# Optimization experiments

Measured on AMD Instinct MI355X. Metric: run time of the kernel, lower is better.

## Reference

```python
import jax, jax.numpy as jnp
import numpy as np

E = 1024  # embedding_dim
H = 64    # head_size

def setup_inputs() -> dict:
    key = jax.random.key(0)
    k1, k2, k3, k4 = jax.random.split(key, 4)
    x = jax.random.normal(k1, (4, 4096, E), dtype=jnp.float32)
    # nn.Linear(E, H, bias=False) weights have shape [H, E]; y = x @ W.T
    s = 1.0 / np.sqrt(E)
    Wq = jax.random.normal(k2, (H, E), dtype=jnp.float32) * s
    Wk = jax.random.normal(k3, (H, E), dtype=jnp.float32) * s
    Wv = jax.random.normal(k4, (H, E), dtype=jnp.float32) * s
    return {"x": x, "Wq": Wq, "Wk": Wk, "Wv": Wv}

def reference(x, Wq, Wk, Wv):
    B, T, E_ = x.shape
    q = jnp.einsum('bte,he->bth', x, Wq)
    k = jnp.einsum('bte,he->bth', x, Wk)
    v = jnp.einsum('bte,he->bth', x, Wv)
    # NOTE: original scales by sqrt(embedding_dim), not head_size
    scores = jnp.einsum('bqh,bkh->bqk', q, k) / jnp.sqrt(jnp.asarray(E_, x.dtype))
    causal = jnp.tril(jnp.ones((T, T), dtype=bool))
    scores = jnp.where(causal, scores, -jnp.inf)
    weights = jax.nn.softmax(scores, axis=-1)
    return jnp.einsum('bqk,bkh->bqh', weights, v)
```

## Files before the change

### kernel.cpp

```cpp
#include <hip/hip_runtime.h>
#include <stdint.h>

typedef __bf16 bf16x8 __attribute__((ext_vector_type(8)));
typedef float  f32x4  __attribute__((ext_vector_type(4)));

#define E_DIM 1024
#define H_DIM 64
#define T_SEQ 4096
#define B_BAT 4
#define M_TOT (B_BAT * T_SEQ)

__device__ __forceinline__ uint32_t f2bf1(float f) {
    uint32_t u = __float_as_uint(f);
    return (u + 0x7FFFu + ((u >> 16) & 1u)) >> 16;
}
__device__ __forceinline__ uint32_t f2bf2(float lo, float hi) {
    return f2bf1(lo) | (f2bf1(hi) << 16);
}
__device__ __forceinline__ bf16x8 ldfrag(const ushort* p) {
    return __builtin_bit_cast(bf16x8, *(const uint4*)p);
}

__global__ __launch_bounds__(256) void wcvt(const float* __restrict__ Wq,
                                            const float* __restrict__ Wk,
                                            const float* __restrict__ Wv,
                                            ushort* __restrict__ Wfm) {
    int g = blockIdx.x * 256 + threadIdx.x;
    int n = g >> 7;
    int k8 = g & 127;
    const float* src = (n < 64) ? (Wq + (size_t)n * E_DIM)
                     : (n < 128) ? (Wk + (size_t)(n - 64) * E_DIM)
                     : (Wv + (size_t)(n - 128) * E_DIM);
    float sc = (n < 64) ? 0.03125f : 1.0f;
    float4 a = *(const float4*)(src + k8 * 8);
    float4 b = *(const float4*)(src + k8 * 8 + 4);
    uint4 o;
    o.x = f2bf2(a.x * sc, a.y * sc); o.y = f2bf2(a.z * sc, a.w * sc);
    o.z = f2bf2(b.x * sc, b.y * sc); o.w = f2bf2(b.z * sc, b.w * sc);
    int s = k8 >> 3, kc = (k8 >> 2) & 1, qd = k8 & 3;
    int nt = n >> 4, lm = n & 15;
    int lane = qd * 16 + lm;
    *(uint4*)(Wfm + (((size_t)(s * 12 + nt) * 2 + kc) * 64 + lane) * 8) = o;
}

__global__ __launch_bounds__(256, 2) void qkv(const float* __restrict__ x,
                                              const ushort* __restrict__ Wfm,
                                              ushort* __restrict__ Qfm,
                                              ushort* __restrict__ Kfm,
                                              ushort* __restrict__ Vfm) {
    __shared__ ushort alds[2][32 * 72];
    __shared__ ushort ldsC[32 * 136];
    __shared__ ushort ldsVt[64 * 40];
    const int tid = threadIdx.x;
    const int w = tid >> 6, l = tid & 63;
    const int lm = l & 15, qd = l >> 4;
    const int m0 = blockIdx.x * 32;

    f32x4 acc[2][3];
#pragma unroll
    for (int r2 = 0; r2 < 2; ++r2)
#pragma unroll
        for (int t = 0; t < 3; ++t) acc[r2][t] = (f32x4){0.f, 0.f, 0.f, 0.f};

    const int srow = tid >> 3, kseg = tid & 7;
    const float* xsrc = x + (size_t)(m0 + srow) * E_DIM + kseg * 8;

    {
        float4 a0 = *(const float4*)xsrc;
        float4 a1 = *(const float4*)(xsrc + 4);
        uint4 u;
        u.x = f2bf2(a0.x, a0.y); u.y = f2bf2(a0.z, a0.w);
        u.z = f2bf2(a1.x, a1.y); u.w = f2bf2(a1.z, a1.w);
        *(uint4*)(&alds[0][srow * 72 + kseg * 8]) = u;
    }
    __syncthreads();

    for (int s = 0; s < 16; ++s) {
        const int cb = s & 1, nb = cb ^ 1;
        const bool pre = s < 15;
        float4 n0, n1;
        if (pre) {
            n0 = *(const float4*)(xsrc + (s + 1) * 64);
            n1 = *(const float4*)(xsrc + (s + 1) * 64 + 4);
        }
        bf16x8 wf[3][2];
#pragma unroll
        for (int t = 0; t < 3; ++t)
#pragma unroll
            for (int kc = 0; kc < 2; ++kc)
                wf[t][kc] = ldfrag(Wfm + (((size_t)(s * 12 + w * 3 + t) * 2 + kc) * 64 + l) * 8);
        bf16x8 af[2][2];
#pragma unroll
        for (int r2 = 0; r2 < 2; ++r2)
#pragma unroll
            for (int kc = 0; kc < 2; ++kc)
                af[r2][kc] = ldfrag(&alds[cb][(r2 * 16 + lm) * 72 + kc * 32 + qd * 8]);
#pragma unroll
        for (int t = 0; t < 3; ++t)
#pragma unroll
            for (int kc = 0; kc < 2; ++kc)
#pragma unroll
                for (int r2 = 0; r2 < 2; ++r2)
                    acc[r2][t] = __builtin_amdgcn_mfma_f32_16x16x32_bf16(af[r2][kc], wf[t][kc], acc[r2][t], 0, 0, 0);
        if (pre) {
            uint4 u;
            u.x = f2bf2(n0.x, n0.y); u.y = f2bf2(n0.z, n0.w);
            u.z = f2bf2(n1.x, n1.y); u.w = f2bf2(n1.z, n1.w);
            *(uint4*)(&alds[nb][srow * 72 + kseg * 8]) = u;
        }
        __syncthreads();
    }

#pragma unroll
    for (int r2 = 0; r2 < 2; ++r2)
#pragma unroll
        for (int t = 0; t < 3; ++t) {
            int gc = w * 48 + t * 16 + lm;
            int m = r2 * 16 + qd * 4;
#pragma unroll
            for (int rr = 0; rr < 4; ++rr) {
                ushort v = (ushort)f2bf1(acc[r2][t][rr]);
                if (gc < 128) ldsC[(m + rr) * 136 + gc] = v;
                else          ldsVt[(gc - 128) * 40 + (m + rr)] = v;
            }
        }
    __syncthreads();

    const int g16b = m0 >> 4;
    const int kt64 = m0 >> 6;
    const int tb   = (m0 >> 4) & 3;
    const int kcv  = (m0 >> 5) & 1;
#pragma unroll
    for (int ii = 0; ii < 3; ++ii) {
        int i = w + ii * 4;
        uint4 val;
        ushort* dst;
        if (i < 4) {
            int qt_l = i >> 1, kc = i & 1;
            val = *(const uint4*)(&ldsC[(qt_l * 16 + lm) * 136 + kc * 32 + qd * 8]);
            dst = Qfm + (((size_t)(g16b + qt_l) * 2 + kc) * 64 + l) * 8;
        } else if (i < 8) {
            int j2 = i - 4, t_l = j2 >> 1, kc = j2 & 1;
            val = *(const uint4*)(&ldsC[(t_l * 16 + lm) * 136 + 64 + kc * 32 + qd * 8]);
            dst = Kfm + (((size_t)((kt64 * 4 + tb + t_l) * 2 + kc)) * 64 + l) * 8;
        } else {
            int t = i - 8;
            val = *(const uint4*)(&ldsVt[(t * 16 + lm) * 40 + qd * 8]);
            dst = Vfm + (((size_t)((kt64 * 4 + t) * 2 + kcv)) * 64 + l) * 8;
        }
        *(uint4*)dst = val;
    }
}

__global__ __launch_bounds__(256, 2) void flash(const ushort* __restrict__ Qfm,
                                                const ushort* __restrict__ Kfm,
                                                const ushort* __restrict__ Vfm,
                                                float* __restrict__ Opart,
                                                float* __restrict__ lpart) {
    __shared__ ushort plds[4][16 * 80];
    const int tid = threadIdx.x;
    const int wv = tid >> 6, l = tid & 63;
    const int lm = l & 15, qd = l >> 4;
    const int pr = blockIdx.x;
    const int bt = blockIdx.y;
    const int h  = blockIdx.z;
    ushort* myp = plds[wv];

#pragma unroll 1
    for (int half = 0; half < 2; ++half) {
        const int qt = half ? (63 - pr) : pr;
        const int qrow = qt * 64 + wv * 16 + lm;
        const size_t rowg = (size_t)bt * T_SEQ + qt * 64 + wv * 16;
        const int g16 = bt * 256 + qt * 4 + wv;

        bf16x8 qf0, qf1;
        {
            const ushort* qp = Qfm + ((size_t)g16 * 2) * 512 + l * 8;
            qf0 = ldfrag(qp);
            qf1 = ldfrag(qp + 512);
        }
        f32x4 o[4];
#pragma unroll
        for (int t = 0; t < 4; ++t) o[t] = (f32x4){0.f, 0.f, 0.f, 0.f};
        float lacc = 0.f;

#pragma unroll 1
        for (int kt = h; kt <= qt; kt += 4) {
            const ushort* kb = Kfm + ((size_t)(bt * 64 + kt) * 8) * 512;
            const ushort* vb = Vfm + ((size_t)(bt * 64 + kt) * 8) * 512;
            f32x4 sf[4];
#pragma unroll
            for (int t = 0; t < 4; ++t) sf[t] = (f32x4){0.f, 0.f, 0.f, 0.f};
#pragma unroll
            for (int t = 0; t < 4; ++t) {
                bf16x8 k0 = ldfrag(kb + (t * 2 + 0) * 512 + l * 8);
                bf16x8 k1 = ldfrag(kb + (t * 2 + 1) * 512 + l * 8);
                sf[t] = __builtin_amdgcn_mfma_f32_16x16x32_bf16(k0, qf0, sf[t], 0, 0, 0);
                sf[t] = __builtin_amdgcn_mfma_f32_16x16x32_bf16(k1, qf1, sf[t], 0, 0, 0);
            }
            uint4 vu[4][2];
#pragma unroll
            for (int t = 0; t < 4; ++t) {
                vu[t][0] = *(const uint4*)(vb + (t * 2 + 0) * 512 + l * 8);
                vu[t][1] = *(const uint4*)(vb + (t * 2 + 1) * 512 + l * 8);
            }
#pragma unroll
            for (int t = 0; t < 4; ++t) {
                int keyb = kt * 64 + t * 16 + qd * 4;
#pragma unroll
                for (int rr = 0; rr < 4; ++rr) {
                    float pe = __expf(sf[t][rr]);
                    if (keyb + rr > qrow) pe = 0.f;
                    lacc += pe;
                    myp[lm * 80 + t * 16 + qd * 4 + rr] = (ushort)f2bf1(pe);
                }
            }
            __builtin_amdgcn_wave_barrier();
            __builtin_amdgcn_s_waitcnt(0xC07F);
            __builtin_amdgcn_wave_barrier();
            bf16x8 pf0 = ldfrag(myp + lm * 80 + qd * 8);
            bf16x8 pf1 = ldfrag(myp + lm * 80 + 32 + qd * 8);
#pragma unroll
            for (int t = 0; t < 4; ++t) {
                bf16x8 v0 = __builtin_bit_cast(bf16x8, vu[t][0]);
                bf16x8 v1 = __builtin_bit_cast(bf16x8, vu[t][1]);
                o[t] = __builtin_amdgcn_mfma_f32_16x16x32_bf16(pf0, v0, o[t], 0, 0, 0);
                o[t] = __builtin_amdgcn_mfma_f32_16x16x32_bf16(pf1, v1, o[t], 0, 0, 0);
            }
            __builtin_amdgcn_wave_barrier();
        }
        lacc += __shfl_xor(lacc, 16);
        lacc += __shfl_xor(lacc, 32);

        float* ob = Opart + ((size_t)h * M_TOT + rowg) * 64;
#pragma unroll
        for (int t = 0; t < 4; ++t)
#pragma unroll
            for (int rr = 0; rr < 4; ++rr)
                ob[(size_t)(qd * 4 + rr) * 64 + t * 16 + lm] = o[t][rr];
        if (qd == 0) lpart[(size_t)h * M_TOT + rowg + lm] = lacc;
    }
}

__global__ __launch_bounds__(256) void combine(const float* __restrict__ Opart,
                                               const float* __restrict__ lpart,
                                               float* __restrict__ out) {
    int i4 = blockIdx.x * 256 + threadIdx.x;
    size_t base = (size_t)i4 * 4;
    int row = i4 >> 4;
    float ls = lpart[row] + lpart[M_TOT + row] + lpart[2 * M_TOT + row] + lpart[3 * M_TOT + row];
    const size_t SP = (size_t)M_TOT * 64;
    float4 a = *(const float4*)(Opart + base);
    float4 b = *(const float4*)(Opart + SP + base);
    float4 c = *(const float4*)(Opart + 2 * SP + base);
    float4 d = *(const float4*)(Opart + 3 * SP + base);
    float inv = 1.0f / ls;
    float4 o;
    o.x = (a.x + b.x + c.x + d.x) * inv;
    o.y = (a.y + b.y + c.y + d.y) * inv;
    o.z = (a.z + b.z + c.z + d.z) * inv;
    o.w = (a.w + b.w + c.w + d.w) * inv;
    *(float4*)(out + base) = o;
}

extern "C" void kernel_launch(void* const* d_in, const int* in_sizes, int n_in,
                              void* d_out, int out_size, void* d_ws, size_t ws_size,
                              hipStream_t stream) {
    const float* x  = (const float*)d_in[0];
    const float* Wq = (const float*)d_in[1];
    const float* Wk = (const float*)d_in[2];
    const float* Wv = (const float*)d_in[3];
    float* out = (float*)d_out;

    char* ws = (char*)d_ws;
    ushort* Wfm = (ushort*)(ws);
    ushort* Qfm = (ushort*)(ws + 393216);
    ushort* Kfm = (ushort*)(ws + 2490368);
    ushort* Vfm = (ushort*)(ws + 4587520);
    float*  Op  = (float*) (ws + 6684672);
    float*  lp  = (float*) (ws + 23461888);

    wcvt<<<96, 256, 0, stream>>>(Wq, Wk, Wv, Wfm);
    qkv<<<512, 256, 0, stream>>>(x, Wfm, Qfm, Kfm, Vfm);
    flash<<<dim3(32, B_BAT, 4), 256, 0, stream>>>(Qfm, Kfm, Vfm, Op, lp);
    combine<<<1024, 256, 0, stream>>>(Op, lp, out);
}
```

Measured before the change: 141.6 us.

## Raise occupancy, deepen x prefetch, specialize causal mask, pack P stores

The QKV kernel now overlays its staging and epilogue shared buffers in a union, raises its launch bound to 3 blocks per CU, and prefetches x two steps ahead, using a waitcnt+barrier helper in place of __syncthreads. The flash kernel raises its launch bound to 4, shrinks the P tile row stride from 80 to 72, and stores P as packed uint2 writes instead of scalar ushort writes. It also skips the per-element causal compare on non-diagonal key tiles and writes zeros for fully masked 16-key sub-tiles. Higher occupancy targets may force register spilling, and the new row pitch may cause LDS bank conflicts.

```diff
diff --git a/kernel.cpp b/kernel.cpp
--- a/kernel.cpp
+++ b/kernel.cpp
@@ -14,11 +14,15 @@
     uint32_t u = __float_as_uint(f);
     return (u + 0x7FFFu + ((u >> 16) & 1u)) >> 16;
 }
-__device__ __forceinline__ uint32_t f2bf2(float lo, float hi) {
+__device__ __forceinline__ uint32_t pk2(float lo, float hi) {
     return f2bf1(lo) | (f2bf1(hi) << 16);
 }
 __device__ __forceinline__ bf16x8 ldfrag(const ushort* p) {
-    return __builtin_bit_cast(bf16x8, *(const uint4*)p);
+    return __builtin_bit_cast(bf16x8, *(const uint4*)(p));
+}
+__device__ __forceinline__ void barrier_lgkm() {
+    __builtin_amdgcn_s_waitcnt(0xC07F);
+    __builtin_amdgcn_s_barrier();
 }
 
 __global__ __launch_bounds__(256) void wcvt(const float* __restrict__ Wq,
@@ -35,22 +39,23 @@
     float4 a = *(const float4*)(src + k8 * 8);
     float4 b = *(const float4*)(src + k8 * 8 + 4);
     uint4 o;
-    o.x = f2bf2(a.x * sc, a.y * sc); o.y = f2bf2(a.z * sc, a.w * sc);
-    o.z = f2bf2(b.x * sc, b.y * sc); o.w = f2bf2(b.z * sc, b.w * sc);
+    o.x = pk2(a.x * sc, a.y * sc); o.y = pk2(a.z * sc, a.w * sc);
+    o.z = pk2(b.x * sc, b.y * sc); o.w = pk2(b.z * sc, b.w * sc);
     int s = k8 >> 3, kc = (k8 >> 2) & 1, qd = k8 & 3;
     int nt = n >> 4, lm = n & 15;
     int lane = qd * 16 + lm;
     *(uint4*)(Wfm + (((size_t)(s * 12 + nt) * 2 + kc) * 64 + lane) * 8) = o;
 }
 
-__global__ __launch_bounds__(256, 2) void qkv(const float* __restrict__ x,
+__global__ __launch_bounds__(256, 3) void qkv(const float* __restrict__ x,
                                               const ushort* __restrict__ Wfm,
                                               ushort* __restrict__ Qfm,
                                               ushort* __restrict__ Kfm,
                                               ushort* __restrict__ Vfm) {
-    __shared__ ushort alds[2][32 * 72];
-    __shared__ ushort ldsC[32 * 136];
-    __shared__ ushort ldsVt[64 * 40];
+    __shared__ union {
+        ushort a[2][32 * 72];
+        struct { ushort c[32 * 136]; ushort vt[64 * 40]; } epi;
+    } sm;
     const int tid = threadIdx.x;
     const int w = tid >> 6, l = tid & 63;
     const int lm = l & 15, qd = l >> 4;
@@ -68,20 +73,19 @@
     {
         float4 a0 = *(const float4*)xsrc;
         float4 a1 = *(const float4*)(xsrc + 4);
-        uint4 u;
-        u.x = f2bf2(a0.x, a0.y); u.y = f2bf2(a0.z, a0.w);
-        u.z = f2bf2(a1.x, a1.y); u.w = f2bf2(a1.z, a1.w);
-        *(uint4*)(&alds[0][srow * 72 + kseg * 8]) = u;
+        uint4 u = {pk2(a0.x, a0.y), pk2(a0.z, a0.w), pk2(a1.x, a1.y), pk2(a1.z, a1.w)};
+        *(uint4*)(&sm.a[0][srow * 72 + kseg * 8]) = u;
     }
+    float4 xn0 = *(const float4*)(xsrc + 64);
+    float4 xn1 = *(const float4*)(xsrc + 68);
     __syncthreads();
 
     for (int s = 0; s < 16; ++s) {
         const int cb = s & 1, nb = cb ^ 1;
-        const bool pre = s < 15;
-        float4 n0, n1;
-        if (pre) {
-            n0 = *(const float4*)(xsrc + (s + 1) * 64);
-            n1 = *(const float4*)(xsrc + (s + 1) * 64 + 4);
+        float4 x20 = xn0, x21 = xn1;
+        if (s < 14) {
+            x20 = *(const float4*)(xsrc + (s + 2) * 64);
+            x21 = *(const float4*)(xsrc + (s + 2) * 64 + 4);
         }
         bf16x8 wf[3][2];
 #pragma unroll
@@ -94,7 +98,7 @@
         for (int r2 = 0; r2 < 2; ++r2)
 #pragma unroll
             for (int kc = 0; kc < 2; ++kc)
-                af[r2][kc] = ldfrag(&alds[cb][(r2 * 16 + lm) * 72 + kc * 32 + qd * 8]);
+                af[r2][kc] = ldfrag(&sm.a[cb][(r2 * 16 + lm) * 72 + kc * 32 + qd * 8]);
 #pragma unroll
         for (int t = 0; t < 3; ++t)
 #pragma unroll
@@ -102,14 +106,14 @@
 #pragma unroll
                 for (int r2 = 0; r2 < 2; ++r2)
                     acc[r2][t] = __builtin_amdgcn_mfma_f32_16x16x32_bf16(af[r2][kc], wf[t][kc], acc[r2][t], 0, 0, 0);
-        if (pre) {
-            uint4 u;
-            u.x = f2bf2(n0.x, n0.y); u.y = f2bf2(n0.z, n0.w);
-            u.z = f2bf2(n1.x, n1.y); u.w = f2bf2(n1.z, n1.w);
-            *(uint4*)(&alds[nb][srow * 72 + kseg * 8]) = u;
-        }
-        __syncthreads();
+        if (s < 15) {
+            uint4 u = {pk2(xn0.x, xn0.y), pk2(xn0.z, xn0.w), pk2(xn1.x, xn1.y), pk2(xn1.z, xn1.w)};
+            *(uint4*)(&sm.a[nb][srow * 72 + kseg * 8]) = u;
+        }
+        xn0 = x20; xn1 = x21;
+        if (s < 15) barrier_lgkm();
     }
+    __syncthreads();
 
 #pragma unroll
     for (int r2 = 0; r2 < 2; ++r2)
@@ -120,8 +124,8 @@
 #pragma unroll
             for (int rr = 0; rr < 4; ++rr) {
                 ushort v = (ushort)f2bf1(acc[r2][t][rr]);
-                if (gc < 128) ldsC[(m + rr) * 136 + gc] = v;
-                else          ldsVt[(gc - 128) * 40 + (m + rr)] = v;
+                if (gc < 128) sm.epi.c[(m + rr) * 136 + gc] = v;
+                else          sm.epi.vt[(gc - 128) * 40 + (m + rr)] = v;
             }
         }
     __syncthreads();
@@ -137,27 +141,27 @@
         ushort* dst;
         if (i < 4) {
             int qt_l = i >> 1, kc = i & 1;
-            val = *(const uint4*)(&ldsC[(qt_l * 16 + lm) * 136 + kc * 32 + qd * 8]);
+            val = *(const uint4*)(&sm.epi.c[(qt_l * 16 + lm) * 136 + kc * 32 + qd * 8]);
             dst = Qfm + (((size_t)(g16b + qt_l) * 2 + kc) * 64 + l) * 8;
         } else if (i < 8) {
             int j2 = i - 4, t_l = j2 >> 1, kc = j2 & 1;
-            val = *(const uint4*)(&ldsC[(t_l * 16 + lm) * 136 + 64 + kc * 32 + qd * 8]);
+            val = *(const uint4*)(&sm.epi.c[(t_l * 16 + lm) * 136 + 64 + kc * 32 + qd * 8]);
             dst = Kfm + (((size_t)((kt64 * 4 + tb + t_l) * 2 + kc)) * 64 + l) * 8;
         } else {
             int t = i - 8;
-            val = *(const uint4*)(&ldsVt[(t * 16 + lm) * 40 + qd * 8]);
+            val = *(const uint4*)(&sm.epi.vt[(t * 16 + lm) * 40 + qd * 8]);
             dst = Vfm + (((size_t)((kt64 * 4 + t) * 2 + kcv)) * 64 + l) * 8;
         }
         *(uint4*)dst = val;
     }
 }
 
-__global__ __launch_bounds__(256, 2) void flash(const ushort* __restrict__ Qfm,
+__global__ __launch_bounds__(256, 4) void flash(const ushort* __restrict__ Qfm,
                                                 const ushort* __restrict__ Kfm,
                                                 const ushort* __restrict__ Vfm,
                                                 float* __restrict__ Opart,
                                                 float* __restrict__ lpart) {
-    __shared__ ushort plds[4][16 * 80];
+    __shared__ ushort plds[4][16 * 72];
     const int tid = threadIdx.x;
     const int wv = tid >> 6, l = tid & 63;
     const int lm = l & 15, qd = l >> 4;
@@ -169,7 +173,6 @@
 #pragma unroll 1
     for (int half = 0; half < 2; ++half) {
         const int qt = half ? (63 - pr) : pr;
-        const int qrow = qt * 64 + wv * 16 + lm;
         const size_t rowg = (size_t)bt * T_SEQ + qt * 64 + wv * 16;
         const int g16 = bt * 256 + qt * 4 + wv;
 
@@ -204,22 +207,43 @@
                 vu[t][0] = *(const uint4*)(vb + (t * 2 + 0) * 512 + l * 8);
                 vu[t][1] = *(const uint4*)(vb + (t * 2 + 1) * 512 + l * 8);
             }
-#pragma unroll
-            for (int t = 0; t < 4; ++t) {
-                int keyb = kt * 64 + t * 16 + qd * 4;
-#pragma unroll
-                for (int rr = 0; rr < 4; ++rr) {
-                    float pe = __expf(sf[t][rr]);
-                    if (keyb + rr > qrow) pe = 0.f;
-                    lacc += pe;
-                    myp[lm * 80 + t * 16 + qd * 4 + rr] = (ushort)f2bf1(pe);
+            ushort* wp = myp + lm * 72 + qd * 4;
+            if (kt != qt) {
+#pragma unroll
+                for (int t = 0; t < 4; ++t) {
+                    float p0 = __expf(sf[t][0]), p1 = __expf(sf[t][1]);
+                    float p2 = __expf(sf[t][2]), p3 = __expf(sf[t][3]);
+                    lacc += (p0 + p1) + (p2 + p3);
+                    *(uint2*)(wp + t * 16) = uint2{pk2(p0, p1), pk2(p2, p3)};
+                }
+            } else {
+#pragma unroll
+                for (int t = 0; t < 4; ++t) {
+                    if (t < wv) {
+                        float p0 = __expf(sf[t][0]), p1 = __expf(sf[t][1]);
+                        float p2 = __expf(sf[t][2]), p3 = __expf(sf[t][3]);
+                        lacc += (p0 + p1) + (p2 + p3);
+                        *(uint2*)(wp + t * 16) = uint2{pk2(p0, p1), pk2(p2, p3)};
+                    } else if (t == wv) {
+                        float p[4];
+#pragma unroll
+                        for (int rr = 0; rr < 4; ++rr) {
+                            float pe = __expf(sf[t][rr]);
+                            if (qd * 4 + rr > lm) pe = 0.f;
+                            lacc += pe;
+                            p[rr] = pe;
+                        }
+                        *(uint2*)(wp + t * 16) = uint2{pk2(p[0], p[1]), pk2(p[2], p[3])};
+                    } else {
+                        *(uint2*)(wp + t * 16) = uint2{0u, 0u};
+                    }
                 }
             }
             __builtin_amdgcn_wave_barrier();
             __builtin_amdgcn_s_waitcnt(0xC07F);
             __builtin_amdgcn_wave_barrier();
-            bf16x8 pf0 = ldfrag(myp + lm * 80 + qd * 8);
-            bf16x8 pf1 = ldfrag(myp + lm * 80 + 32 + qd * 8);
+            bf16x8 pf0 = ldfrag(myp + lm * 72 + qd * 8);
+            bf16x8 pf1 = ldfrag(myp + lm * 72 + 32 + qd * 8);
 #pragma unroll
             for (int t = 0; t < 4; ++t) {
                 bf16x8 v0 = __builtin_bit_cast(bf16x8, vu[t][0]);
```

New measurement: 135.8 us. 4.0% less time.
